# Kernel optimization log

Measured on AMD Instinct MI355X. Metric: run time of the kernel, lower is better.

Reference implementation:

```python
import jax, jax.numpy as jnp
import numpy as np

N, E = 3000, 96000
IN_C, HID, OUT_C = 512, 256, 64
K1, K2, K3 = 2000, 1000, 500  # ceil(ratio * n) per depth; ratios = [2000/N, 0.5, 0.5]


def gcn_conv(A, x, W, b):
    # GCNConv(improved=True): A_hat = A + 2I, symmetric norm; A[i, j] = weight of edge j -> i
    n = A.shape[0]
    Ah = A + 2.0 * jnp.eye(n, dtype=A.dtype)
    deg = Ah.sum(axis=1)
    dis = jnp.where(deg > 0, jax.lax.rsqrt(deg), 0.0)
    return (dis[:, None] * Ah * dis[None, :]) @ (x @ W) + b


def augment(A):
    # GraphUNet.augment_adj: add self loops, A @ A (spspmm), remove self loops
    n = A.shape[0]
    eye = jnp.eye(n, dtype=A.dtype)
    Ah = A + eye
    return (Ah @ Ah) * (1.0 - eye)


def topk_pool(A, x, w, k):
    # TopKPooling: score = tanh((x @ w) / ||w||); keep top-k nodes, scale feats, take sub-adjacency
    score = jnp.tanh((x @ w) / jnp.linalg.norm(w))
    sv, perm = jax.lax.top_k(score, k)
    return x[perm] * sv[:, None], A[perm][:, perm], perm


def setup_inputs():
    key = jax.random.key(0)
    ks = jax.random.split(key, 16)

    def glorot(k, shape):
        lim = float(np.sqrt(6.0 / (shape[0] + shape[1])))
        return jax.random.uniform(k, shape, jnp.float32, -lim, lim)

    return {
        "x": jax.random.normal(ks[0], (N, IN_C), jnp.float32),
        "edge_index": jax.random.randint(ks[1], (2, E), 0, N, jnp.int32),
        "W0": glorot(ks[2], (IN_C, HID)), "b0": jnp.zeros((HID,), jnp.float32),
        "W1": glorot(ks[3], (HID, HID)), "b1": jnp.zeros((HID,), jnp.float32),
        "W2": glorot(ks[4], (HID, HID)), "b2": jnp.zeros((HID,), jnp.float32),
        "W3": glorot(ks[5], (HID, HID)), "b3": jnp.zeros((HID,), jnp.float32),
        "p1": jax.random.normal(ks[6], (HID,), jnp.float32),
        "p2": jax.random.normal(ks[7], (HID,), jnp.float32),
        "p3": jax.random.normal(ks[8], (HID,), jnp.float32),
        "U0": glorot(ks[9], (HID, HID)), "c0": jnp.zeros((HID,), jnp.float32),
        "U1": glorot(ks[10], (HID, HID)), "c1": jnp.zeros((HID,), jnp.float32),
        "U2": glorot(ks[11], (HID, OUT_C)), "c2": jnp.zeros((OUT_C,), jnp.float32),
    }


def reference(x, edge_index, W0, b0, W1, b1, W2, b2, W3, b3, p1, p2, p3, U0, c0, U1, c1, U2, c2):
    # eval mode: dropout_edge(p=0.2) and F.dropout(p=0.92) are identity
    relu = jax.nn.relu
    src, dst = edge_index[0], edge_index[1]
    A = jnp.zeros((N, N), x.dtype).at[dst, src].add(1.0)  # dense adjacency, coalesces duplicates

    x0 = relu(gcn_conv(A, x, W0, b0))                     # down conv 0 on original graph
    x1in, A1, perm1 = topk_pool(augment(A), x0, p1, K1)
    x1 = relu(gcn_conv(A1, x1in, W1, b1))
    x2in, A2, perm2 = topk_pool(augment(A1), x1, p2, K2)
    x2 = relu(gcn_conv(A2, x2in, W2, b2))
    x3in, A3, perm3 = topk_pool(augment(A2), x2, p3, K3)
    x3 = relu(gcn_conv(A3, x3in, W3, b3))

    h = x2 + jnp.zeros_like(x2).at[perm3].set(x3)         # unpool + sum residual
    h = relu(gcn_conv(A2, h, U0, c0))
    h = x1 + jnp.zeros_like(x1).at[perm2].set(h)
    h = relu(gcn_conv(A1, h, U1, c1))
    h = x0 + jnp.zeros_like(x0).at[perm1].set(h)
    h = gcn_conv(A, h, U2, c2)                            # final up conv, no activation
    return jax.nn.log_softmax(h, axis=1)
```

## Files before the change

### kernel.cpp

```cpp
#include <hip/hip_runtime.h>
#include <math.h>
#include <stdint.h>

#define N0   3000
#define NE   96000
#define INC  512
#define HIDF 256
#define OUTC 64
#define KP1  2000
#define KP2  1000
#define KP3  500
#define KP1P 2048
#define KP2P 1024
#define KP3P 512

typedef __bf16 bf16x8 __attribute__((ext_vector_type(8)));
typedef float f32x4 __attribute__((ext_vector_type(4)));

#define GLDS16(gp, lp)                                                   \
  __builtin_amdgcn_global_load_lds(                                      \
      (__attribute__((address_space(1))) void*)(gp),                     \
      (__attribute__((address_space(3))) void*)(lp), 16, 0, 0)

static __global__ void count_k(const int* __restrict__ ei, int* __restrict__ cd) {
  int e = blockIdx.x * blockDim.x + threadIdx.x;
  if (e < NE) atomicAdd(&cd[ei[NE + e]], 1);
}

static __global__ __launch_bounds__(1024) void scan_excl_k(const int* __restrict__ cnt,
                                                           int* __restrict__ start, int n) {
  __shared__ int s[4096];
  int tid = threadIdx.x;
  for (int i = tid; i < 4096; i += blockDim.x) s[i] = (i < n) ? cnt[i] : 0;
  __syncthreads();
  for (int d = 1; d < 4096; d <<= 1) {
    int v[4]; int r = 0;
    for (int i = tid; i < 4096; i += blockDim.x, ++r) v[r] = (i >= d) ? s[i - d] : 0;
    __syncthreads();
    r = 0;
    for (int i = tid; i < 4096; i += blockDim.x, ++r) s[i] += v[r];
    __syncthreads();
  }
  for (int i = tid; i < n; i += blockDim.x) start[i] = (i == 0) ? 0 : s[i - 1];
  if (tid == 0) start[n] = s[n - 1];
}

static __global__ void scatter_k(const int* __restrict__ ei, const int* __restrict__ sd,
                                 int* __restrict__ fd, int* __restrict__ bd) {
  int e = blockIdx.x * blockDim.x + threadIdx.x;
  if (e < NE) {
    int d = ei[NE + e];
    bd[sd[d] + atomicAdd(&fd[d], 1)] = ei[e];
  }
}

static __global__ void dis0_k(const int* __restrict__ cd, float* __restrict__ dis0) {
  int i = blockIdx.x * blockDim.x + threadIdx.x;
  if (i < N0) dis0[i] = rsqrtf((float)cd[i] + 2.0f);
}

static __global__ __launch_bounds__(256) void augA_masked_k(
    const int* __restrict__ st, const int* __restrict__ bk,
    const int* __restrict__ perm, const int* __restrict__ pos,
    float* __restrict__ A1, __bf16* __restrict__ A1bf, float* __restrict__ dis1) {
  __shared__ float row[KP1];
  __shared__ float sh[4];
  int tid = threadIdx.x, lane = tid & 63, wave = tid >> 6;
  int r = blockIdx.x;
  int vi = perm[r];
  for (int c = tid; c < KP1; c += 256) row[c] = 0.f;
  __syncthreads();
  int b = st[vi], e = st[vi + 1];
  for (int t = b + wave; t < e; t += 4) {
    int k = bk[t];
    int jb = st[k], je = st[k + 1];
    for (int u = jb + lane; u < je; u += 64) {
      int p = pos[bk[u]];
      if (p >= 0) atomicAdd(&row[p], 1.0f);
    }
  }
  if (wave == 0)
    for (int t = b + lane; t < e; t += 64) {
      int p = pos[bk[t]];
      if (p >= 0) atomicAdd(&row[p], 2.0f);
    }
  __syncthreads();
  if (tid == 0) row[r] = 0.f;
  __syncthreads();
  float s = 0.f;
  for (int c = tid; c < KP1P; c += 256) {
    float v = (c < KP1) ? row[c] : 0.f;
    if (c < KP1) A1[(size_t)r * KP1 + c] = v;
    A1bf[(size_t)r * KP1P + c] = (__bf16)v;
    s += v;
  }
#pragma unroll
  for (int o = 32; o > 0; o >>= 1) s += __shfl_down(s, o, 64);
  if (lane == 0) sh[wave] = s;
  __syncthreads();
  if (tid == 0) dis1[r] = rsqrtf(sh[0] + sh[1] + sh[2] + sh[3] + 2.0f);
}

static __global__ void spmm_sc_k(const int* __restrict__ start, const int* __restrict__ idx,
                                 const float* __restrict__ xw, const float* __restrict__ dis,
                                 float* __restrict__ out, int F) {
  int row = blockIdx.x;
  int b = start[row], e = start[row + 1];
  int f = threadIdx.x;
  __shared__ int nb[256];
  __shared__ float nd[256];
  float acc = 0.f;
  for (int t0 = b; t0 < e; t0 += blockDim.x) {
    int m = min((int)blockDim.x, e - t0);
    __syncthreads();
    if (f < m) { int s = idx[t0 + f]; nb[f] = s; nd[f] = dis[s]; }
    __syncthreads();
    for (int t = 0; t < m; ++t) acc += xw[(size_t)nb[t] * F + f] * nd[t];
  }
  out[(size_t)row * F + f] = acc;
}

static __global__ void conv_hilo_k(const float* __restrict__ in, int R, int C, int Cp,
                                   __bf16* __restrict__ oh, __bf16* __restrict__ ol) {
  int idx = blockIdx.x * blockDim.x + threadIdx.x;
  if (idx < R * Cp) {
    int r = idx / Cp, c = idx - r * Cp;
    float v = (c < C) ? in[(size_t)r * C + c] : 0.f;
    __bf16 h = (__bf16)v;
    oh[idx] = h;
    if (ol) ol[idx] = (__bf16)(v - (float)h);
  }
}

static __global__ __launch_bounds__(256) void tconv_k(const float* __restrict__ in, int R, int C, int Rp,
                                                      __bf16* __restrict__ oh, __bf16* __restrict__ ol) {
  __shared__ float t[32][33];
  int r0 = blockIdx.x * 32, c0 = blockIdx.y * 32;
  int lr = threadIdx.x >> 5, lc = threadIdx.x & 31;
#pragma unroll
  for (int i = 0; i < 4; ++i) {
    int r = r0 + lr + i * 8, c = c0 + lc;
    t[lr + i * 8][lc] = (r < R && c < C) ? in[(size_t)r * C + c] : 0.f;
  }
  __syncthreads();
#pragma unroll
  for (int i = 0; i < 4; ++i) {
    int c = c0 + lr + i * 8, r = r0 + lc;
    if (c < C) {
      float v = t[lc][lr + i * 8];
      __bf16 h = (__bf16)v;
      oh[(size_t)c * Rp + r] = h;
      if (ol) ol[(size_t)c * Rp + r] = (__bf16)(v - (float)h);
    }
  }
}

static __global__ __launch_bounds__(256) void redtconv_k(const float* __restrict__ Cp, int ks, int mn,
                                                         int R, int C, int Rp,
                                                         __bf16* __restrict__ oh, __bf16* __restrict__ ol,
                                                         const float* __restrict__ disv,
                                                         float* __restrict__ xw_out) {
  __shared__ float t[32][33];
  int r0 = blockIdx.x * 32, c0 = blockIdx.y * 32;
  int lr = threadIdx.x >> 5, lc = threadIdx.x & 31;
#pragma unroll
  for (int i = 0; i < 4; ++i) {
    int r = r0 + lr + i * 8, c = c0 + lc;
    float v = 0.f;
    if (r < R && c < C) {
      size_t idx = (size_t)r * C + c;
      for (int z = 0; z < ks; ++z) v += Cp[(size_t)z * mn + idx];
      xw_out[idx] = v;
    }
    t[lr + i * 8][lc] = v;
  }
  __syncthreads();
#pragma unroll
  for (int i = 0; i < 4; ++i) {
    int c = c0 + lr + i * 8, r = r0 + lc;
    if (c < C) {
      float v = t[lc][lr + i * 8];
      if (r < R) v *= disv[r];
      __bf16 h = (__bf16)v;
      oh[(size_t)c * Rp + r] = h;
      ol[(size_t)c * Rp + r] = (__bf16)(v - (float)h);
    }
  }
}

static __global__ void grows2_k(const __bf16* __restrict__ s1, const __bf16* __restrict__ s2,
                                const int* __restrict__ perm, __bf16* __restrict__ d1,
                                __bf16* __restrict__ d2, int k, int L) {
  int idx = blockIdx.x * blockDim.x + threadIdx.x;
  int nv = L >> 3;
  if (idx < k * nv) {
    int r = idx / nv, c8 = (idx - r * nv) << 3;
    int sr = perm[r];
    bf16x8 v1 = *(const bf16x8*)(s1 + (size_t)sr * L + c8);
    bf16x8 v2 = *(const bf16x8*)(s2 + (size_t)sr * L + c8);
    if (sr >= c8 && sr < c8 + 8) v2[sr - c8] = (__bf16)((float)v2[sr - c8] + 2.0f);
    *(bf16x8*)(d1 + (size_t)r * L + c8) = v1;
    *(bf16x8*)(d2 + (size_t)r * L + c8) = v2;
  }
}

static __global__ void grows4_k(const __bf16* __restrict__ ah, const __bf16* __restrict__ al,
                                const __bf16* __restrict__ bh, const __bf16* __restrict__ bl,
                                const int* __restrict__ perm,
                                __bf16* __restrict__ dah, __bf16* __restrict__ dal,
                                __bf16* __restrict__ dbh, __bf16* __restrict__ dbl,
                                int k, int L) {
  int idx = blockIdx.x * blockDim.x + threadIdx.x;
  int nv = L >> 3;
  if (idx < k * nv) {
    int r = idx / nv, c8 = (idx - r * nv) << 3;
    int sr = perm[r];
    bf16x8 vah = *(const bf16x8*)(ah + (size_t)sr * L + c8);
    bf16x8 val = *(const bf16x8*)(al + (size_t)sr * L + c8);
    bf16x8 vbh = *(const bf16x8*)(bh + (size_t)sr * L + c8);
    bf16x8 vbl = *(const bf16x8*)(bl + (size_t)sr * L + c8);
    if (sr >= c8 && sr < c8 + 8) {
      int e = sr - c8;
      float v = (float)vbh[e] + (float)vbl[e] + 2.0f;
      __bf16 h = (__bf16)v;
      vbh[e] = h;
      vbl[e] = (__bf16)(v - (float)h);
    }
    *(bf16x8*)(dah + (size_t)r * L + c8) = vah;
    *(bf16x8*)(dal + (size_t)r * L + c8) = val;
    *(bf16x8*)(dbh + (size_t)r * L + c8) = vbh;
    *(bf16x8*)(dbl + (size_t)r * L + c8) = vbl;
  }
}

static __global__ void ghilo_k(const float* __restrict__ src, const int* __restrict__ perm,
                               const float* __restrict__ sv, __bf16* __restrict__ oh,
                               __bf16* __restrict__ ol, int k) {
  int idx = blockIdx.x * blockDim.x + threadIdx.x;
  if (idx < k * HIDF) {
    int r = idx >> 8;
    float v = src[(size_t)perm[r] * HIDF + (idx & 255)] * sv[r];
    __bf16 h = (__bf16)v;
    oh[idx] = h;
    ol[idx] = (__bf16)(v - (float)h);
  }
}

template <int BM, int BN>
static __global__ __launch_bounds__(256) void mgemm_k(
    const __bf16* __restrict__ A0, const __bf16* __restrict__ A1g, const __bf16* __restrict__ A2g,
    const __bf16* __restrict__ B0, const __bf16* __restrict__ B1g, const __bf16* __restrict__ B2g,
    int nseg, float* __restrict__ Cp, int M, int N, int Kp, int kchunk) {
  constexpr int FM = BM / 32, FN = BN / 32;
  __shared__ __bf16 As[2][BM * 64];
  __shared__ __bf16 Bs[2][BN * 64];
  int tid = threadIdx.x;
  int lane = tid & 63, wave = tid >> 6;
  int wx = wave & 1, wy = wave >> 1;
  int l15 = lane & 15, l4 = lane >> 4;
  int brow = blockIdx.y * BM, bcol = blockIdx.x * BN;
  int wrow = wy * (BM / 2), wcol = wx * (BN / 2);
  int srow = lane >> 3, slot = lane & 7;
  int k_beg = blockIdx.z * kchunk;
  int ksteps = kchunk >> 6;
  int nsteps = nseg * ksteps;
  const __bf16* segA[3] = {A0, A1g, A2g};
  const __bf16* segB[3] = {B0, B1g, B2g};

  auto stage = [&](int buf, int t) {
    int seg = t / ksteps;
    int k0 = k_beg + ((t - seg * ksteps) << 6);
    const __bf16* Ag = segA[seg];
    const __bf16* Bg = segB[seg];
#pragma unroll
    for (int i = 0; i < BM / 32; ++i) {
      int rl = (i * 4 + wave) * 8 + srow;
      int gr = brow + rl;
      if (gr >= M) gr = M - 1;
      int col = k0 + ((slot ^ (rl & 7)) << 3);
      GLDS16(Ag + (size_t)gr * Kp + col, &As[buf][(i * 4 + wave) * 8 * 64]);
    }
#pragma unroll
    for (int i = 0; i < BN / 32; ++i) {
      int rl = (i * 4 + wave) * 8 + srow;
      int gc = bcol + rl;
      if (gc >= N) gc = N - 1;
      int col = k0 + ((slot ^ (rl & 7)) << 3);
      GLDS16(Bg + (size_t)gc * Kp + col, &Bs[buf][(i * 4 + wave) * 8 * 64]);
    }
  };

  f32x4 acc[FM][FN] = {};
  stage(0, 0);
  __syncthreads();
  int cur = 0;
  for (int t = 0; t < nsteps; ++t) {
    if (t + 1 < nsteps) stage(cur ^ 1, t + 1);
#pragma unroll
    for (int sub = 0; sub < 2; ++sub) {
      bf16x8 af[FM], bfv[FN];
#pragma unroll
      for (int i = 0; i < FM; ++i) {
        int r = wrow + i * 16 + l15;
        af[i] = *(const bf16x8*)(&As[cur][r * 64 + (((sub * 4 + l4) ^ (r & 7)) << 3)]);
      }
#pragma unroll
      for (int j = 0; j < FN; ++j) {
        int r = wcol + j * 16 + l15;
        bfv[j] = *(const bf16x8*)(&Bs[cur][r * 64 + (((sub * 4 + l4) ^ (r & 7)) << 3)]);
      }
#pragma unroll
      for (int i = 0; i < FM; ++i)
#pragma unroll
        for (int j = 0; j < FN; ++j)
          acc[i][j] = __builtin_amdgcn_mfma_f32_16x16x32_bf16(af[i], bfv[j], acc[i][j], 0, 0, 0);
    }
    __syncthreads();
    cur ^= 1;
  }
  size_t zoff = (size_t)blockIdx.z * M * N;
#pragma unroll
  for (int i = 0; i < FM; ++i)
#pragma unroll
    for (int j = 0; j < FN; ++j) {
      int col = bcol + wcol + j * 16 + l15;
      if (col < N) {
#pragma unroll
        for (int q = 0; q < 4; ++q) {
          int row = brow + wrow + i * 16 + l4 * 4 + q;
          if (row < M) Cp[zoff + (size_t)row * N + col] = acc[i][j][q];
        }
      }
    }
}

static __global__ void reduce_k(const float* __restrict__ p, int ks, int mn, float* __restrict__ out) {
  int idx = blockIdx.x * blockDim.x + threadIdx.x;
  if (idx < mn) {
    float s = 0.f;
    for (int z = 0; z < ks; ++z) s += p[(size_t)z * mn + idx];
    out[idx] = s;
  }
}

static __global__ void conv_epi_k(const float* __restrict__ zp, int ks, int mn,
                                  const float* __restrict__ xw, const float* __restrict__ dis,
                                  const float* __restrict__ b, float* __restrict__ out,
                                  int n, int f, int relu) {
  int idx = blockIdx.x * blockDim.x + threadIdx.x;
  if (idx < n * f) {
    float zv = 0.f;
    for (int z = 0; z < ks; ++z) zv += zp[(size_t)z * mn + idx];
    int i = idx / f, j = idx - i * f;
    float di = dis[i];
    float v = di * zv + 2.0f * di * di * xw[idx] + b[j];
    if (relu) v = fmaxf(v, 0.0f);
    out[idx] = v;
  }
}

static __global__ __launch_bounds__(256) void aug_epi_k(const float* __restrict__ Cp, int ks, int mn,
                                                        int n, int Kpad, float* __restrict__ Af,
                                                        __bf16* __restrict__ bh, __bf16* __restrict__ bl,
                                                        float* __restrict__ dis) {
  __shared__ float sh[4];
  int r = blockIdx.x;
  int tid = threadIdx.x, lane = tid & 63, wave = tid >> 6;
  float ssum = 0.f;
  for (int c = tid; c < Kpad; c += 256) {
    float v = 0.f;
    if (c < n && c != r)
      for (int z = 0; z < ks; ++z) v += Cp[(size_t)z * mn + (size_t)r * n + c];
    if (c < n) Af[(size_t)r * n + c] = v;
    __bf16 h = (__bf16)v;
    bh[(size_t)r * Kpad + c] = h;
    bl[(size_t)r * Kpad + c] = (__bf16)(v - (float)h);
    ssum += v;
  }
#pragma unroll
  for (int o = 32; o > 0; o >>= 1) ssum += __shfl_down(ssum, o, 64);
  if (lane == 0) sh[wave] = ssum;
  __syncthreads();
  if (tid == 0) dis[r] = rsqrtf(sh[0] + sh[1] + sh[2] + sh[3] + 2.0f);
}

static __global__ void score_k(const float* __restrict__ x, const float* __restrict__ w,
                               float* __restrict__ sc, int f) {
  int row = blockIdx.x;
  float s = 0.f, q = 0.f;
  for (int j = threadIdx.x; j < f; j += blockDim.x) {
    float wv = w[j];
    q += wv * wv;
    s += x[(size_t)row * f + j] * wv;
  }
  __shared__ float sh[8], sh2[8];
  int lane = threadIdx.x & 63, wid = threadIdx.x >> 6;
#pragma unroll
  for (int o = 32; o > 0; o >>= 1) { s += __shfl_down(s, o, 64); q += __shfl_down(q, o, 64); }
  if (lane == 0) { sh[wid] = s; sh2[wid] = q; }
  __syncthreads();
  if (threadIdx.x == 0) {
    float t = 0.f, t2 = 0.f;
    int nw = (blockDim.x + 63) >> 6;
    for (int w2 = 0; w2 < nw; ++w2) { t += sh[w2]; t2 += sh2[w2]; }
    sc[row] = tanhf(t / sqrtf(t2));
  }
}

static __global__ __launch_bounds__(256) void topk_rank_k(const float* __restrict__ sc, int n, int k,
                                                          int* __restrict__ perm, float* __restrict__ sv,
                                                          int* __restrict__ pos) {
  __shared__ float s[N0 + 8];
  int tid = threadIdx.x, lane = tid & 63, wave = tid >> 6;
  for (int i = tid; i < n; i += 256) s[i] = sc[i];
  __syncthreads();
  int i = blockIdx.x * 4 + wave;
  if (i < n) {
    float si = s[i];
    int rank = 0;
    for (int j = lane; j < n; j += 64) {
      float sj = s[j];
      rank += (sj > si) || (sj == si && j < i);
    }
#pragma unroll
    for (int o = 32; o > 0; o >>= 1) rank += __shfl_down(rank, o, 64);
    if (lane == 0) {
      pos[i] = (rank < k) ? rank : -1;
      if (rank < k) { perm[rank] = i; sv[rank] = si; }
    }
  }
}

static __global__ void unpool_hilo_k(const float* __restrict__ base, const float* __restrict__ up,
                                     const int* __restrict__ pos, __bf16* __restrict__ oh,
                                     __bf16* __restrict__ ol, int n) {
  int idx = blockIdx.x * blockDim.x + threadIdx.x;
  if (idx < n * HIDF) {
    int i = idx >> 8;
    int p = pos[i];
    float v = base[idx] + (p >= 0 ? up[(size_t)p * HIDF + (idx & 255)] : 0.f);
    __bf16 h = (__bf16)v;
    oh[idx] = h;
    ol[idx] = (__bf16)(v - (float)h);
  }
}

static __global__ void log_softmax_k(const float* __restrict__ h, float* __restrict__ out, int f) {
  int row = blockIdx.x;
  int j = threadIdx.x;
  float vv = h[row * f + j];
  float m = vv;
#pragma unroll
  for (int o = 32; o > 0; o >>= 1) m = fmaxf(m, __shfl_xor(m, o, 64));
  float e = expf(vv - m), s = e;
#pragma unroll
  for (int o = 32; o > 0; o >>= 1) s += __shfl_xor(s, o, 64);
  out[row * f + j] = vv - m - logf(s);
}

extern "C" void kernel_launch(void* const* d_in, const int* in_sizes, int n_in,
                              void* d_out, int out_size, void* d_ws, size_t ws_size,
                              hipStream_t stream) {
  const float* x  = (const float*)d_in[0];
  const int* ei   = (const int*)d_in[1];
  const float* W0 = (const float*)d_in[2];
  const float* b0 = (const float*)d_in[3];
  const float* W1 = (const float*)d_in[4];
  const float* b1 = (const float*)d_in[5];
  const float* W2 = (const float*)d_in[6];
  const float* b2 = (const float*)d_in[7];
  const float* W3 = (const float*)d_in[8];
  const float* b3 = (const float*)d_in[9];
  const float* p1 = (const float*)d_in[10];
  const float* p2 = (const float*)d_in[11];
  const float* p3 = (const float*)d_in[12];
  const float* U0 = (const float*)d_in[13];
  const float* c0 = (const float*)d_in[14];
  const float* U1 = (const float*)d_in[15];
  const float* c1 = (const float*)d_in[16];
  const float* U2 = (const float*)d_in[17];
  const float* c2 = (const float*)d_in[18];
  (void)in_sizes; (void)n_in; (void)out_size; (void)ws_size;

  char* basep = (char*)d_ws;
  size_t off = 0;
  auto alloc = [&](size_t bytes) {
    void* p = basep + off;
    off += (bytes + 255) & ~(size_t)255;
    return p;
  };

  float* A1  = (float*)alloc((size_t)KP1 * KP1 * 4);
  float* A2  = (float*)alloc((size_t)KP2 * KP2 * 4);
  float* A3  = (float*)alloc((size_t)KP3 * KP3 * 4);
  float* xw  = (float*)alloc((size_t)N0 * HIDF * 4);
  float* zb  = (float*)alloc((size_t)N0 * HIDF * 4);
  float* x0  = (float*)alloc((size_t)N0 * HIDF * 4);
  float* x1  = (float*)alloc((size_t)KP1 * HIDF * 4);
  float* x2  = (float*)alloc((size_t)KP2 * HIDF * 4);
  float* x3  = (float*)alloc((size_t)KP3 * HIDF * 4);
  float* hb  = (float*)alloc((size_t)N0 * HIDF * 4);
  float* xfin = (float*)alloc((size_t)N0 * OUTC * 4);
  float* Cpart = (float*)alloc((size_t)36 * 1024 * 1024);
  __bf16* bfAh = (__bf16*)alloc((size_t)N0 * INC * 2);
  __bf16* bfAl = (__bf16*)alloc((size_t)N0 * INC * 2);
  __bf16* bfBh = (__bf16*)alloc((size_t)HIDF * KP1P * 2);
  __bf16* bfBl = (__bf16*)alloc((size_t)HIDF * KP1P * 2);
  __bf16* A1bf  = (__bf16*)alloc((size_t)KP1 * KP1P * 2);
  __bf16* A1tbf = (__bf16*)alloc((size_t)KP1 * KP1P * 2);
  __bf16* Ag    = (__bf16*)alloc((size_t)KP2 * KP1P * 2);
  __bf16* Bg    = (__bf16*)alloc((size_t)KP2 * KP1P * 2);
  __bf16* A2bh  = (__bf16*)alloc((size_t)KP2 * KP2P * 2);
  __bf16* A2bl  = (__bf16*)alloc((size_t)KP2 * KP2P * 2);
  __bf16* A2tbh = (__bf16*)alloc((size_t)KP2 * KP2P * 2);
  __bf16* A2tbl = (__bf16*)alloc((size_t)KP2 * KP2P * 2);
  __bf16* Agh   = (__bf16*)alloc((size_t)KP3 * KP2P * 2);
  __bf16* Agl   = (__bf16*)alloc((size_t)KP3 * KP2P * 2);
  __bf16* Bgh   = (__bf16*)alloc((size_t)KP3 * KP2P * 2);
  __bf16* Bgl   = (__bf16*)alloc((size_t)KP3 * KP2P * 2);
  __bf16* A3bh  = (__bf16*)alloc((size_t)KP3 * KP3P * 2);
  __bf16* A3bl  = (__bf16*)alloc((size_t)KP3 * KP3P * 2);
  float* sc   = (float*)alloc(N0 * 4);
  float* sv   = (float*)alloc(KP1 * 4);
  int* perm1  = (int*)alloc(KP1 * 4);
  int* perm2  = (int*)alloc(KP2 * 4);
  int* perm3  = (int*)alloc(KP3 * 4);
  int* pos1   = (int*)alloc(N0 * 4);
  int* pos2   = (int*)alloc(KP1 * 4);
  int* pos3   = (int*)alloc(KP2 * 4);
  float* dis0 = (float*)alloc(N0 * 4);
  float* dis1 = (float*)alloc(KP1 * 4);
  float* dis2 = (float*)alloc(KP2 * 4);
  float* dis3 = (float*)alloc(KP3 * 4);
  int* cnt_d  = (int*)alloc(N0 * 4);
  int* st_d   = (int*)alloc((N0 + 4) * 4);
  int* fl_d   = (int*)alloc(N0 * 4);
  int* bk_d   = (int*)alloc(NE * 4);

  auto mg = [&](int bm, const __bf16* a0, const __bf16* a1, const __bf16* a2,
                const __bf16* bb0, const __bf16* bb1, const __bf16* bb2,
                int nseg, float* Cp, int M, int N, int Kp, int ks, int kchunk) {
    if (bm == 128) {
      dim3 g((N + 127) / 128, (M + 127) / 128, ks);
      mgemm_k<128, 128><<<g, 256, 0, stream>>>(a0, a1, a2, bb0, bb1, bb2, nseg, Cp, M, N, Kp, kchunk);
    } else {
      dim3 g((N + 63) / 64, (M + 63) / 64, ks);
      mgemm_k<64, 64><<<g, 256, 0, stream>>>(a0, a1, a2, bb0, bb1, bb2, nseg, Cp, M, N, Kp, kchunk);
    }
  };

  auto wgemm = [&](const float* W, int fin, int fout, int n, int bm, int ks, int kchunk) {
    int Kp = (fin + 63) & ~63;
    dim3 tg(Kp / 32, (fout + 31) / 32);
    tconv_k<<<tg, 256, 0, stream>>>(W, fin, fout, Kp, bfBh, bfBl);
    mg(bm, bfAh, bfAh, bfAl, bfBh, bfBl, bfBh, 3, Cpart, n, fout, Kp, ks, kchunk);
  };

  auto prop = [&](int ksw, const __bf16* Abh, const __bf16* Abl, int asegs, int n, int Kp, int bm,
                  int ks, int kchunk, const float* disv, const float* bias, float* outx, int relu) {
    dim3 tg(Kp / 32, HIDF / 32);
    redtconv_k<<<tg, 256, 0, stream>>>(Cpart, ksw, n * HIDF, n, HIDF, Kp, bfBh, bfBl, disv, xw);
    if (asegs == 1) mg(bm, Abh, Abh, nullptr, bfBh, bfBl, nullptr, 2, Cpart, n, HIDF, Kp, ks, kchunk);
    else            mg(bm, Abh, Abh, Abl, bfBh, bfBl, bfBh, 3, Cpart, n, HIDF, Kp, ks, kchunk);
    conv_epi_k<<<(n * HIDF + 255) / 256, 256, 0, stream>>>(Cpart, ks, n * HIDF, xw, disv, bias,
                                                           outx, n, HIDF, relu);
  };

  auto pool = [&](const float* xfeat, int n, const float* p, int k, int* perm, int* pos) {
    score_k<<<n, 256, 0, stream>>>(xfeat, p, sc, HIDF);
    topk_rank_k<<<(n + 3) / 4, 256, 0, stream>>>(sc, n, k, perm, sv, pos);
  };

  hipMemsetAsync(cnt_d, 0, N0 * 4, stream);
  hipMemsetAsync(fl_d, 0, N0 * 4, stream);
  count_k<<<(NE + 255) / 256, 256, 0, stream>>>(ei, cnt_d);
  scan_excl_k<<<1, 1024, 0, stream>>>(cnt_d, st_d, N0);
  scatter_k<<<(NE + 255) / 256, 256, 0, stream>>>(ei, st_d, fl_d, bk_d);
  dis0_k<<<(N0 + 255) / 256, 256, 0, stream>>>(cnt_d, dis0);

  conv_hilo_k<<<((size_t)N0 * INC + 255) / 256, 256, 0, stream>>>(x, N0, INC, INC, bfAh, bfAl);
  wgemm(W0, INC, HIDF, N0, 64, 4, 128);
  reduce_k<<<(N0 * HIDF + 255) / 256, 256, 0, stream>>>(Cpart, 4, N0 * HIDF, xw);
  spmm_sc_k<<<N0, HIDF, 0, stream>>>(st_d, bk_d, xw, dis0, zb, HIDF);
  conv_epi_k<<<(N0 * HIDF + 255) / 256, 256, 0, stream>>>(zb, 1, 0, xw, dis0, b0, x0, N0, HIDF, 1);

  pool(x0, N0, p1, KP1, perm1, pos1);
  augA_masked_k<<<KP1, 256, 0, stream>>>(st_d, bk_d, perm1, pos1, A1, A1bf, dis1);

  ghilo_k<<<((size_t)KP1 * HIDF + 255) / 256, 256, 0, stream>>>(x0, perm1, sv, bfAh, bfAl, KP1);
  wgemm(W1, HIDF, HIDF, KP1, 64, 4, 64);
  prop(4, A1bf, nullptr, 1, KP1, KP1P, 128, 16, 128, dis1, b1, x1, 1);

  pool(x1, KP1, p2, KP2, perm2, pos2);
  {
    dim3 tg(KP1P / 32, (KP1 + 31) / 32);
    tconv_k<<<tg, 256, 0, stream>>>(A1, KP1, KP1, KP1P, A1tbf, nullptr);
  }
  grows2_k<<<((size_t)KP2 * (KP1P / 8) + 255) / 256, 256, 0, stream>>>(A1bf, A1tbf, perm2, Ag, Bg,
                                                                       KP2, KP1P);
  mg(128, Ag, nullptr, nullptr, Bg, nullptr, nullptr, 1, Cpart, KP2, KP2, KP1P, 8, 256);
  aug_epi_k<<<KP2, 256, 0, stream>>>(Cpart, 8, KP2 * KP2, KP2, KP2P, A2, A2bh, A2bl, dis2);

  ghilo_k<<<((size_t)KP2 * HIDF + 255) / 256, 256, 0, stream>>>(x1, perm2, sv, bfAh, bfAl, KP2);
  wgemm(W2, HIDF, HIDF, KP2, 64, 4, 64);
  prop(4, A2bh, A2bl, 2, KP2, KP2P, 64, 8, 128, dis2, b2, x2, 1);

  pool(x2, KP2, p3, KP3, perm3, pos3);
  {
    dim3 tg(KP2P / 32, (KP2 + 31) / 32);
    tconv_k<<<tg, 256, 0, stream>>>(A2, KP2, KP2, KP2P, A2tbh, A2tbl);
  }
  grows4_k<<<((size_t)KP3 * (KP2P / 8) + 255) / 256, 256, 0, stream>>>(
      A2bh, A2bl, A2tbh, A2tbl, perm3, Agh, Agl, Bgh, Bgl, KP3, KP2P);
  mg(64, Agh, Agh, Agl, Bgh, Bgl, Bgh, 3, Cpart, KP3, KP3, KP2P, 8, 128);
  aug_epi_k<<<KP3, 256, 0, stream>>>(Cpart, 8, KP3 * KP3, KP3, KP3P, A3, A3bh, A3bl, dis3);

  ghilo_k<<<((size_t)KP3 * HIDF + 255) / 256, 256, 0, stream>>>(x2, perm3, sv, bfAh, bfAl, KP3);
  wgemm(W3, HIDF, HIDF, KP3, 64, 4, 64);
  prop(4, A3bh, A3bl, 2, KP3, KP3P, 64, 8, 64, dis3, b3, x3, 1);

  unpool_hilo_k<<<(KP2 * HIDF + 255) / 256, 256, 0, stream>>>(x2, x3, pos3, bfAh, bfAl, KP2);
  wgemm(U0, HIDF, HIDF, KP2, 64, 4, 64);
  prop(4, A2bh, A2bl, 2, KP2, KP2P, 64, 8, 128, dis2, c0, hb, 1);

  unpool_hilo_k<<<(KP1 * HIDF + 255) / 256, 256, 0, stream>>>(x1, hb, pos2, bfAh, bfAl, KP1);
  wgemm(U1, HIDF, HIDF, KP1, 64, 4, 64);
  prop(4, A1bf, nullptr, 1, KP1, KP1P, 128, 16, 128, dis1, c1, hb, 1);

  unpool_hilo_k<<<(N0 * HIDF + 255) / 256, 256, 0, stream>>>(x0, hb, pos1, bfAh, bfAl, N0);
  wgemm(U2, HIDF, OUTC, N0, 64, 4, 64);
  reduce_k<<<(N0 * OUTC + 255) / 256, 256, 0, stream>>>(Cpart, 4, N0 * OUTC, xw);
  spmm_sc_k<<<N0, OUTC, 0, stream>>>(st_d, bk_d, xw, dis0, zb, OUTC);
  conv_epi_k<<<(N0 * OUTC + 255) / 256, 256, 0, stream>>>(zb, 1, 0, xw, dis0, c2, xfin, N0, OUTC, 0);

  log_softmax_k<<<N0, 64, 0, stream>>>(xfin, (float*)d_out, OUTC);
}
```

Before: 471.8 us.

## Batch weight conversions, drop fp32 adjacency copies, fuse epilogues, retune GEMM splits

```diff
diff --git a/kernel.cpp b/kernel.cpp
--- a/kernel.cpp
+++ b/kernel.cpp
@@ -28,7 +28,8 @@
 }
 
 static __global__ __launch_bounds__(1024) void scan_excl_k(const int* __restrict__ cnt,
-                                                           int* __restrict__ start, int n) {
+                                                           int* __restrict__ start, int n,
+                                                           float* __restrict__ dis0) {
   __shared__ int s[4096];
   int tid = threadIdx.x;
   for (int i = tid; i < 4096; i += blockDim.x) s[i] = (i < n) ? cnt[i] : 0;
@@ -41,7 +42,10 @@
     for (int i = tid; i < 4096; i += blockDim.x, ++r) s[i] += v[r];
     __syncthreads();
   }
-  for (int i = tid; i < n; i += blockDim.x) start[i] = (i == 0) ? 0 : s[i - 1];
+  for (int i = tid; i < n; i += blockDim.x) {
+    start[i] = (i == 0) ? 0 : s[i - 1];
+    dis0[i] = rsqrtf((float)cnt[i] + 2.0f);
+  }
   if (tid == 0) start[n] = s[n - 1];
 }
 
@@ -54,15 +58,10 @@
   }
 }
 
-static __global__ void dis0_k(const int* __restrict__ cd, float* __restrict__ dis0) {
-  int i = blockIdx.x * blockDim.x + threadIdx.x;
-  if (i < N0) dis0[i] = rsqrtf((float)cd[i] + 2.0f);
-}
-
 static __global__ __launch_bounds__(256) void augA_masked_k(
     const int* __restrict__ st, const int* __restrict__ bk,
     const int* __restrict__ perm, const int* __restrict__ pos,
-    float* __restrict__ A1, __bf16* __restrict__ A1bf, float* __restrict__ dis1) {
+    __bf16* __restrict__ A1bf, float* __restrict__ dis1) {
   __shared__ float row[KP1];
   __shared__ float sh[4];
   int tid = threadIdx.x, lane = tid & 63, wave = tid >> 6;
@@ -90,7 +89,6 @@
   float s = 0.f;
   for (int c = tid; c < KP1P; c += 256) {
     float v = (c < KP1) ? row[c] : 0.f;
-    if (c < KP1) A1[(size_t)r * KP1 + c] = v;
     A1bf[(size_t)r * KP1P + c] = (__bf16)v;
     s += v;
   }
@@ -132,25 +130,53 @@
   }
 }
 
-static __global__ __launch_bounds__(256) void tconv_k(const float* __restrict__ in, int R, int C, int Rp,
-                                                      __bf16* __restrict__ oh, __bf16* __restrict__ ol) {
+struct TDesc { const float* in; __bf16* oh; __bf16* ol; int R, C, Rp; };
+struct TDescs { TDesc d[7]; };
+static __global__ __launch_bounds__(256) void wtconv_k(TDescs ds) {
+  TDesc d = ds.d[blockIdx.z];
+  int r0 = blockIdx.x * 32, c0 = blockIdx.y * 32;
+  if (r0 >= d.Rp || c0 >= d.C) return;
   __shared__ float t[32][33];
+  int lr = threadIdx.x >> 5, lc = threadIdx.x & 31;
+#pragma unroll
+  for (int i = 0; i < 4; ++i) {
+    int r = r0 + lr + i * 8, c = c0 + lc;
+    t[lr + i * 8][lc] = (r < d.R && c < d.C) ? d.in[(size_t)r * d.C + c] : 0.f;
+  }
+  __syncthreads();
+#pragma unroll
+  for (int i = 0; i < 4; ++i) {
+    int c = c0 + lr + i * 8, r = r0 + lc;
+    if (c < d.C) {
+      float v = t[lc][lr + i * 8];
+      __bf16 h = (__bf16)v;
+      d.oh[(size_t)c * d.Rp + r] = h;
+      d.ol[(size_t)c * d.Rp + r] = (__bf16)(v - (float)h);
+    }
+  }
+}
+
+static __global__ __launch_bounds__(256) void btrans_k(const __bf16* __restrict__ ih,
+                                                       const __bf16* __restrict__ il,
+                                                       __bf16* __restrict__ oh, __bf16* __restrict__ ol,
+                                                       int Rin, int Ls, int Cout, int Lo) {
+  __shared__ __bf16 th[32][40], tl[32][40];
   int r0 = blockIdx.x * 32, c0 = blockIdx.y * 32;
   int lr = threadIdx.x >> 5, lc = threadIdx.x & 31;
 #pragma unroll
   for (int i = 0; i < 4; ++i) {
     int r = r0 + lr + i * 8, c = c0 + lc;
-    t[lr + i * 8][lc] = (r < R && c < C) ? in[(size_t)r * C + c] : 0.f;
+    bool ok = (r < Rin);
+    th[lr + i * 8][lc] = ok ? ih[(size_t)r * Ls + c] : (__bf16)0.f;
+    if (il) tl[lr + i * 8][lc] = ok ? il[(size_t)r * Ls + c] : (__bf16)0.f;
   }
   __syncthreads();
 #pragma unroll
   for (int i = 0; i < 4; ++i) {
     int c = c0 + lr + i * 8, r = r0 + lc;
-    if (c < C) {
-      float v = t[lc][lr + i * 8];
-      __bf16 h = (__bf16)v;
-      oh[(size_t)c * Rp + r] = h;
-      if (ol) ol[(size_t)c * Rp + r] = (__bf16)(v - (float)h);
+    if (c < Cout) {
+      oh[(size_t)c * Lo + r] = th[lc][lr + i * 8];
+      if (ol) ol[(size_t)c * Lo + r] = tl[lc][lr + i * 8];
     }
   }
 }
@@ -360,7 +386,7 @@
 }
 
 static __global__ __launch_bounds__(256) void aug_epi_k(const float* __restrict__ Cp, int ks, int mn,
-                                                        int n, int Kpad, float* __restrict__ Af,
+                                                        int n, int Kpad,
                                                         __bf16* __restrict__ bh, __bf16* __restrict__ bl,
                                                         float* __restrict__ dis) {
   __shared__ float sh[4];
@@ -371,7 +397,6 @@
     float v = 0.f;
     if (c < n && c != r)
       for (int z = 0; z < ks; ++z) v += Cp[(size_t)z * mn + (size_t)r * n + c];
-    if (c < n) Af[(size_t)r * n + c] = v;
     __bf16 h = (__bf16)v;
     bh[(size_t)r * Kpad + c] = h;
     bl[(size_t)r * Kpad + c] = (__bf16)(v - (float)h);
@@ -445,17 +470,19 @@
   }
 }
 
-static __global__ void log_softmax_k(const float* __restrict__ h, float* __restrict__ out, int f) {
-  int row = blockIdx.x;
-  int j = threadIdx.x;
-  float vv = h[row * f + j];
-  float m = vv;
+static __global__ void epilsm_k(const float* __restrict__ zb, const float* __restrict__ xw,
+                                const float* __restrict__ dis, const float* __restrict__ b,
+                                float* __restrict__ out) {
+  int r = blockIdx.x, j = threadIdx.x;
+  float di = dis[r];
+  float v = di * zb[r * OUTC + j] + 2.0f * di * di * xw[r * OUTC + j] + b[j];
+  float m = v;
 #pragma unroll
   for (int o = 32; o > 0; o >>= 1) m = fmaxf(m, __shfl_xor(m, o, 64));
-  float e = expf(vv - m), s = e;
+  float e = expf(v - m), s = e;
 #pragma unroll
   for (int o = 32; o > 0; o >>= 1) s += __shfl_xor(s, o, 64);
-  out[row * f + j] = vv - m - logf(s);
+  out[r * OUTC + j] = v - m - logf(s);
 }
 
 extern "C" void kernel_launch(void* const* d_in, const int* in_sizes, int n_in,
@@ -490,9 +517,6 @@
     return p;
   };
 
-  float* A1  = (float*)alloc((size_t)KP1 * KP1 * 4);
-  float* A2  = (float*)alloc((size_t)KP2 * KP2 * 4);
-  float* A3  = (float*)alloc((size_t)KP3 * KP3 * 4);
   float* xw  = (float*)alloc((size_t)N0 * HIDF * 4);
   float* zb  = (float*)alloc((size_t)N0 * HIDF * 4);
   float* x0  = (float*)alloc((size_t)N0 * HIDF * 4);
@@ -500,8 +524,7 @@
   float* x2  = (float*)alloc((size_t)KP2 * HIDF * 4);
   float* x3  = (float*)alloc((size_t)KP3 * HIDF * 4);
   float* hb  = (float*)alloc((size_t)N0 * HIDF * 4);
-  float* xfin = (float*)alloc((size_t)N0 * OUTC * 4);
-  float* Cpart = (float*)alloc((size_t)36 * 1024 * 1024);
+  float* Cpart = (float*)alloc((size_t)20 * 1024 * 1024);
   __bf16* bfAh = (__bf16*)alloc((size_t)N0 * INC * 2);
   __bf16* bfAl = (__bf16*)alloc((size_t)N0 * INC * 2);
   __bf16* bfBh = (__bf16*)alloc((size_t)HIDF * KP1P * 2);
@@ -520,6 +543,20 @@
   __bf16* Bgl   = (__bf16*)alloc((size_t)KP3 * KP2P * 2);
   __bf16* A3bh  = (__bf16*)alloc((size_t)KP3 * KP3P * 2);
   __bf16* A3bl  = (__bf16*)alloc((size_t)KP3 * KP3P * 2);
+  __bf16* w0h = (__bf16*)alloc((size_t)HIDF * 512 * 2);
+  __bf16* w0l = (__bf16*)alloc((size_t)HIDF * 512 * 2);
+  __bf16* w1h = (__bf16*)alloc((size_t)HIDF * 256 * 2);
+  __bf16* w1l = (__bf16*)alloc((size_t)HIDF * 256 * 2);
+  __bf16* w2h = (__bf16*)alloc((size_t)HIDF * 256 * 2);
+  __bf16* w2l = (__bf16*)alloc((size_t)HIDF * 256 * 2);
+  __bf16* w3h = (__bf16*)alloc((size_t)HIDF * 256 * 2);
+  __bf16* w3l = (__bf16*)alloc((size_t)HIDF * 256 * 2);
+  __bf16* u0h = (__bf16*)alloc((size_t)HIDF * 256 * 2);
+  __bf16* u0l = (__bf16*)alloc((size_t)HIDF * 256 * 2);
+  __bf16* u1h = (__bf16*)alloc((size_t)HIDF * 256 * 2);
+  __bf16* u1l = (__bf16*)alloc((size_t)HIDF * 256 * 2);
+  __bf16* u2h = (__bf16*)alloc((size_t)OUTC * 256 * 2);
+  __bf16* u2l = (__bf16*)alloc((size_t)OUTC * 256 * 2);
   float* sc   = (float*)alloc(N0 * 4);
   float* sv   = (float*)alloc(KP1 * 4);
   int* perm1  = (int*)alloc(KP1 * 4);
@@ -532,36 +569,36 @@
   float* dis1 = (float*)alloc(KP1 * 4);
   float* dis2 = (float*)alloc(KP2 * 4);
   float* dis3 = (float*)alloc(KP3 * 4);
-  int* cnt_d  = (int*)alloc(N0 * 4);
+  int* cf     = (int*)alloc((size_t)2 * 3072 * 4);
+  int* cnt_d  = cf;
+  int* fl_d   = cf + 3072;
   int* st_d   = (int*)alloc((N0 + 4) * 4);
-  int* fl_d   = (int*)alloc(N0 * 4);
   int* bk_d   = (int*)alloc(NE * 4);
 
-  auto mg = [&](int bm, const __bf16* a0, const __bf16* a1, const __bf16* a2,
+  auto mg = [&](int bm, int bn, const __bf16* a0, const __bf16* a1, const __bf16* a2,
                 const __bf16* bb0, const __bf16* bb1, const __bf16* bb2,
-                int nseg, float* Cp, int M, int N, int Kp, int ks, int kchunk) {
-    if (bm == 128) {
-      dim3 g((N + 127) / 128, (M + 127) / 128, ks);
-      mgemm_k<128, 128><<<g, 256, 0, stream>>>(a0, a1, a2, bb0, bb1, bb2, nseg, Cp, M, N, Kp, kchunk);
-    } else {
-      dim3 g((N + 63) / 64, (M + 63) / 64, ks);
-      mgemm_k<64, 64><<<g, 256, 0, stream>>>(a0, a1, a2, bb0, bb1, bb2, nseg, Cp, M, N, Kp, kchunk);
-    }
+                int nseg, int M, int N, int Kp, int ks, int kchunk) {
+    dim3 g((N + bn - 1) / bn, (M + bm - 1) / bm, ks);
+    if (bm == 128 && bn == 128)
+      mgemm_k<128, 128><<<g, 256, 0, stream>>>(a0, a1, a2, bb0, bb1, bb2, nseg, Cpart, M, N, Kp, kchunk);
+    else if (bm == 128)
+      mgemm_k<128, 64><<<g, 256, 0, stream>>>(a0, a1, a2, bb0, bb1, bb2, nseg, Cpart, M, N, Kp, kchunk);
+    else
+      mgemm_k<64, 64><<<g, 256, 0, stream>>>(a0, a1, a2, bb0, bb1, bb2, nseg, Cpart, M, N, Kp, kchunk);
   };
 
-  auto wgemm = [&](const float* W, int fin, int fout, int n, int bm, int ks, int kchunk) {
+  auto wgemm = [&](const __bf16* wh, const __bf16* wl, int fin, int fout, int n, int bm,
+                   int ks, int kchunk) {
     int Kp = (fin + 63) & ~63;
-    dim3 tg(Kp / 32, (fout + 31) / 32);
-    tconv_k<<<tg, 256, 0, stream>>>(W, fin, fout, Kp, bfBh, bfBl);
-    mg(bm, bfAh, bfAh, bfAl, bfBh, bfBl, bfBh, 3, Cpart, n, fout, Kp, ks, kchunk);
+    mg(bm, 64, bfAh, bfAh, bfAl, wh, wl, wh, 3, n, fout, Kp, ks, kchunk);
   };
 
   auto prop = [&](int ksw, const __bf16* Abh, const __bf16* Abl, int asegs, int n, int Kp, int bm,
                   int ks, int kchunk, const float* disv, const float* bias, float* outx, int relu) {
     dim3 tg(Kp / 32, HIDF / 32);
     redtconv_k<<<tg, 256, 0, stream>>>(Cpart, ksw, n * HIDF, n, HIDF, Kp, bfBh, bfBl, disv, xw);
-    if (asegs == 1) mg(bm, Abh, Abh, nullptr, bfBh, bfBl, nullptr, 2, Cpart, n, HIDF, Kp, ks, kchunk);
-    else            mg(bm, Abh, Abh, Abl, bfBh, bfBl, bfBh, 3, Cpart, n, HIDF, Kp, ks, kchunk);
+    if (asegs == 1) mg(bm, 64, Abh, Abh, nullptr, bfBh, bfBl, nullptr, 2, n, HIDF, Kp, ks, kchunk);
+    else            mg(bm, 64, Abh, Abh, Abl, bfBh, bfBl, bfBh, 3, n, HIDF, Kp, ks, kchunk);
     conv_epi_k<<<(n * HIDF + 255) / 256, 256, 0, stream>>>(Cpart, ks, n * HIDF, xw, disv, bias,
                                                            outx, n, HIDF, relu);
   };
@@ -571,67 +608,70 @@
     topk_rank_k<<<(n + 3) / 4, 256, 0, stream>>>(sc, n, k, perm, sv, pos);
   };
 
-  hipMemsetAsync(cnt_d, 0, N0 * 4, stream);
-  hipMemsetAsync(fl_d, 0, N0 * 4, stream);
+  hipMemsetAsync(cf, 0, (size_t)2 * 3072 * 4, stream);
   count_k<<<(NE + 255) / 256, 256, 0, stream>>>(ei, cnt_d);
-  scan_excl_k<<<1, 1024, 0, stream>>>(cnt_d, st_d, N0);
+  {
+    TDescs ds;
+    ds.d[0] = {W0, w0h, w0l, INC, HIDF, 512};
+    ds.d[1] = {W1, w1h, w1l, HIDF, HIDF, 256};
+    ds.d[2] = {W2, w2h, w2l, HIDF, HIDF, 256};
+    ds.d[3] = {W3, w3h, w3l, HIDF, HIDF, 256};
+    ds.d[4] = {U0, u0h, u0l, HIDF, HIDF, 256};
+    ds.d[5] = {U1, u1h, u1l, HIDF, HIDF, 256};
+    ds.d[6] = {U2, u2h, u2l, HIDF, OUTC, 256};
+    wtconv_k<<<dim3(16, 8, 7), 256, 0, stream>>>(ds);
+  }
+  scan_excl_k<<<1, 1024, 0, stream>>>(cnt_d, st_d, N0, dis0);
   scatter_k<<<(NE + 255) / 256, 256, 0, stream>>>(ei, st_d, fl_d, bk_d);
-  dis0_k<<<(N0 + 255) / 256, 256, 0, stream>>>(cnt_d, dis0);
 
   conv_hilo_k<<<((size_t)N0 * INC + 255) / 256, 256, 0, stream>>>(x, N0, INC, INC, bfAh, bfAl);
-  wgemm(W0, INC, HIDF, N0, 64, 4, 128);
+  wgemm(w0h, w0l, INC, HIDF, N0, 128, 4, 128);
   reduce_k<<<(N0 * HIDF + 255) / 256, 256, 0, stream>>>(Cpart, 4, N0 * HIDF, xw);
   spmm_sc_k<<<N0, HIDF, 0, stream>>>(st_d, bk_d, xw, dis0, zb, HIDF);
   conv_epi_k<<<(N0 * HIDF + 255) / 256, 256, 0, stream>>>(zb, 1, 0, xw, dis0, b0, x0, N0, HIDF, 1);
 
   pool(x0, N0, p1, KP1, perm1, pos1);
-  augA_masked_k<<<KP1, 256, 0, stream>>>(st_d, bk_d, perm1, pos1, A1, A1bf, dis1);
+  augA_masked_k<<<KP1, 256, 0, stream>>>(st_d, bk_d, perm1, pos1, A1bf, dis1);
 
   ghilo_k<<<((size_t)KP1 * HIDF + 255) / 256, 256, 0, stream>>>(x0, perm1, sv, bfAh, bfAl, KP1);
-  wgemm(W1, HIDF, HIDF, KP1, 64, 4, 64);
-  prop(4, A1bf, nullptr, 1, KP1, KP1P, 128, 16, 128, dis1, b1, x1, 1);
+  wgemm(w1h, w1l, HIDF, HIDF, KP1, 128, 4, 64);
+  prop(4, A1bf, nullptr, 1, KP1, KP1P, 128, 4, 512, dis1, b1, x1, 1);
 
   pool(x1, KP1, p2, KP2, perm2, pos2);
-  {
-    dim3 tg(KP1P / 32, (KP1 + 31) / 32);
-    tconv_k<<<tg, 256, 0, stream>>>(A1, KP1, KP1, KP1P, A1tbf, nullptr);
-  }
+  btrans_k<<<dim3(KP1P / 32, (KP1 + 31) / 32), 256, 0, stream>>>(A1bf, nullptr, A1tbf, nullptr,
+                                                                 KP1, KP1P, KP1, KP1P);
   grows2_k<<<((size_t)KP2 * (KP1P / 8) + 255) / 256, 256, 0, stream>>>(A1bf, A1tbf, perm2, Ag, Bg,
                                                                        KP2, KP1P);
-  mg(128, Ag, nullptr, nullptr, Bg, nullptr, nullptr, 1, Cpart, KP2, KP2, KP1P, 8, 256);
-  aug_epi_k<<<KP2, 256, 0, stream>>>(Cpart, 8, KP2 * KP2, KP2, KP2P, A2, A2bh, A2bl, dis2);
+  mg(128, 128, Ag, nullptr, nullptr, Bg, nullptr, nullptr, 1, KP2, KP2, KP1P, 4, 512);
+  aug_epi_k<<<KP2, 256, 0, stream>>>(Cpart, 4, KP2 * KP2, KP2, KP2P, A2bh, A2bl, dis2);
 
   ghilo_k<<<((size_t)KP2 * HIDF + 255) / 256, 256, 0, stream>>>(x1, perm2, sv, bfAh, bfAl, KP2);
-  wgemm(W2, HIDF, HIDF, KP2, 64, 4, 64);
-  prop(4, A2bh, A2bl, 2, KP2, KP2P, 64, 8, 128, dis2, b2, x2, 1);
+  wgemm(w2h, w2l, HIDF, HIDF, KP2, 64, 4, 64);
+  prop(4, A2bh, A2bl, 2, KP2, KP2P, 128, 8, 128, dis2, b2, x2, 1);
 
   pool(x2, KP2, p3, KP3, perm3, pos3);
-  {
-    dim3 tg(KP2P / 32, (KP2 + 31) / 32);
-    tconv_k<<<tg, 256, 0, stream>>>(A2, KP2, KP2, KP2P, A2tbh, A2tbl);
-  }
+  btrans_k<<<dim3(KP2P / 32, (KP2 + 31) / 32), 256, 0, stream>>>(A2bh, A2bl, A2tbh, A2tbl,
+                                                                 KP2, KP2P, KP2, KP2P);
   grows4_k<<<((size_t)KP3 * (KP2P / 8) + 255) / 256, 256, 0, stream>>>(
       A2bh, A2bl, A2tbh, A2tbl, perm3, Agh, Agl, Bgh, Bgl, KP3, KP2P);
-  mg(64, Agh, Agh, Agl, Bgh, Bgl, Bgh, 3, Cpart, KP3, KP3, KP2P, 8, 128);
-  aug_epi_k<<<KP3, 256, 0, stream>>>(Cpart, 8, KP3 * KP3, KP3, KP3P, A3, A3bh, A3bl, dis3);
+  mg(64, 64, Agh, Agh, Agl, Bgh, Bgl, Bgh, 3, KP3, KP3, KP2P, 4, 256);
+  aug_epi_k<<<KP3, 256, 0, stream>>>(Cpart, 4, KP3 * KP3, KP3, KP3P, A3bh, A3bl, dis3);
 
   ghilo_k<<<((size_t)KP3 * HIDF + 255) / 256, 256, 0, stream>>>(x2, perm3, sv, bfAh, bfAl, KP3);
-  wgemm(W3, HIDF, HIDF, KP3, 64, 4, 64);
+  wgemm(w3h, w3l, HIDF, HIDF, KP3, 64, 4, 64);
   prop(4, A3bh, A3bl, 2, KP3, KP3P, 64, 8, 64, dis3, b3, x3, 1);
 
   unpool_hilo_k<<<(KP2 * HIDF + 255) / 256, 256, 0, stream>>>(x2, x3, pos3, bfAh, bfAl, KP2);
-  wgemm(U0, HIDF, HIDF, KP2, 64, 4, 64);
-  prop(4, A2bh, A2bl, 2, KP2, KP2P, 64, 8, 128, dis2, c0, hb, 1);
+  wgemm(u0h, u0l, HIDF, HIDF, KP2, 64, 4, 64);
+  prop(4, A2bh, A2bl, 2, KP2, KP2P, 128, 8, 128, dis2, c0, hb, 1);
 
   unpool_hilo_k<<<(KP1 * HIDF + 255) / 256, 256, 0, stream>>>(x1, hb, pos2, bfAh, bfAl, KP1);
-  wgemm(U1, HIDF, HIDF, KP1, 64, 4, 64);
-  prop(4, A1bf, nullptr, 1, KP1, KP1P, 128, 16, 128, dis1, c1, hb, 1);
+  wgemm(u1h, u1l, HIDF, HIDF, KP1, 128, 4, 64);
+  prop(4, A1bf, nullptr, 1, KP1, KP1P, 128, 4, 512, dis1, c1, hb, 1);
 
   unpool_hilo_k<<<(N0 * HIDF + 255) / 256, 256, 0, stream>>>(x0, hb, pos1, bfAh, bfAl, N0);
-  wgemm(U2, HIDF, OUTC, N0, 64, 4, 64);
+  wgemm(u2h, u2l, HIDF, OUTC, N0, 64, 4, 64);
   reduce_k<<<(N0 * OUTC + 255) / 256, 256, 0, stream>>>(Cpart, 4, N0 * OUTC, xw);
   spmm_sc_k<<<N0, OUTC, 0, stream>>>(st_d, bk_d, xw, dis0, zb, OUTC);
-  conv_epi_k<<<(N0 * OUTC + 255) / 256, 256, 0, stream>>>(zb, 1, 0, xw, dis0, c2, xfin, N0, OUTC, 0);
-
-  log_softmax_k<<<N0, 64, 0, stream>>>(xfin, (float*)d_out, OUTC);
-}
+  epilsm_k<<<N0, OUTC, 0, stream>>>(zb, xw, dis0, c2, (float*)d_out);
+}
```

Measured after the change: 450.1 us. 4.6% less time.
